# Kernel optimization log

Measured on AMD Instinct MI355X. Metric: run time of the kernel, lower is better.

The kernel has to match this reference:

```python
import jax, jax.numpy as jnp
import numpy as np

N = 20000
NNBR = 64
MESH = (64, 64, 64)
ORDER = 4          # B-spline interpolation order
ALPHA = 0.35       # Ewald splitting parameter (1/Angstrom)
BOX = 73.68        # cubic box edge (Angstrom)
KE = 14.399645478425668  # Coulomb constant, eV*Angstrom/e^2


def _Mn(x, n):
    """Cardinal B-spline M_n(x), support [0, n]."""
    if n == 2:
        return jnp.maximum(0.0, 1.0 - jnp.abs(x - 1.0))
    return (x * _Mn(x, n - 1) + (n - x) * _Mn(x - 1.0, n - 1)) / (n - 1)


def _bspline_fac(K):
    """|b(m)|^-2 ... i.e. 1/|Euler spline denominator|^2 per mesh dim."""
    m = jnp.arange(K, dtype=jnp.float32)
    k = jnp.arange(ORDER - 1, dtype=jnp.float32)
    Mv = _Mn(k + 1.0, ORDER)                       # M_n(1..n-1)
    phase = 2.0 * jnp.pi * m[:, None] * k[None, :] / K
    dre = jnp.sum(Mv * jnp.cos(phase), axis=1)
    dim = jnp.sum(Mv * jnp.sin(phase), axis=1)
    return 1.0 / (dre * dre + dim * dim)


def _pme_energy(positions, charges, cell, nbr, shifts):
    n = positions.shape[0]
    # ---------------- real-space short-range sum ----------------
    i_idx = jnp.arange(n)[:, None]
    valid = (nbr >= 0) & ~((nbr == i_idx) & jnp.all(shifts == 0, axis=-1))
    j = jnp.where(nbr >= 0, nbr, 0)
    rvec = positions[j] + shifts.astype(positions.dtype) @ cell - positions[:, None, :]
    r2 = jnp.sum(rvec * rvec, axis=-1)
    r = jnp.sqrt(jnp.where(valid, r2, 1.0))
    qq = charges[:, None] * charges[j]
    e_real = 0.5 * jnp.sum(jnp.where(valid, qq * jax.scipy.special.erfc(ALPHA * r) / r, 0.0))
    # ---------------- B-spline charge spreading ----------------
    Kx, Ky, Kz = MESH
    frac = positions @ jnp.linalg.inv(cell)        # cell rows = lattice vectors
    u = frac * jnp.array(MESH, dtype=positions.dtype)
    base = jnp.floor(u)
    t = u - base                                   # in [0, 1)
    basei = base.astype(jnp.int32)
    offs = jnp.arange(ORDER)
    wx = _Mn(t[:, 0:1] + offs, ORDER)              # [N, ORDER]
    wy = _Mn(t[:, 1:2] + offs, ORDER)
    wz = _Mn(t[:, 2:3] + offs, ORDER)
    ix = (basei[:, 0:1] - offs) % Kx
    iy = (basei[:, 1:2] - offs) % Ky
    iz = (basei[:, 2:3] - offs) % Kz
    W = (charges[:, None] * wx)[:, :, None, None] * wy[:, None, :, None] * wz[:, None, None, :]
    IDX = (ix[:, :, None, None] * Ky + iy[:, None, :, None]) * Kz + iz[:, None, None, :]
    mesh = jnp.zeros(Kx * Ky * Kz, positions.dtype).at[IDX.reshape(-1)].add(W.reshape(-1)).reshape(MESH)
    # ---------------- reciprocal-space FFT convolution ----------------
    Q = jnp.fft.fftn(mesh)
    Brec = 2.0 * jnp.pi * jnp.linalg.inv(cell).T   # rows are reciprocal vectors
    mx = (jnp.fft.fftfreq(Kx) * Kx).astype(positions.dtype)
    my = (jnp.fft.fftfreq(Ky) * Ky).astype(positions.dtype)
    mz = (jnp.fft.fftfreq(Kz) * Kz).astype(positions.dtype)
    kvec = (mx[:, None, None, None] * Brec[0] + my[None, :, None, None] * Brec[1]
            + mz[None, None, :, None] * Brec[2])
    k2 = jnp.sum(kvec * kvec, axis=-1)
    a2 = ALPHA * ALPHA
    kern = jnp.where(k2 > 0, jnp.exp(-k2 / (4.0 * a2)) / jnp.where(k2 > 0, k2, 1.0), 0.0)
    C = _bspline_fac(Kx)[:, None, None] * _bspline_fac(Ky)[None, :, None] * _bspline_fac(Kz)[None, None, :]
    vol = jnp.abs(jnp.linalg.det(cell))
    e_rec = (2.0 * jnp.pi / vol) * jnp.sum(kern * C * (Q.real ** 2 + Q.imag ** 2))
    # ---------------- self + neutralizing background ----------------
    qtot = jnp.sum(charges)
    e_self = -(ALPHA / jnp.sqrt(jnp.pi)) * jnp.sum(charges * charges)
    e_bg = -(jnp.pi / (2.0 * a2 * vol)) * qtot * qtot
    return e_real + e_rec + e_self + e_bg


def setup_inputs() -> dict:
    key = jax.random.key(0)
    k1, k2, k3 = jax.random.split(key, 3)
    positions = jax.random.uniform(k1, (N, 3), jnp.float32) * BOX
    q = jax.random.normal(k2, (N,), jnp.float32)
    q = q - jnp.mean(q)  # neutral system
    cell = BOX * jnp.eye(3, dtype=jnp.float32)
    nbr = jax.random.randint(k3, (N, NNBR), 0, N, jnp.int32)
    shifts = jnp.zeros((N, NNBR, 3), jnp.int32)
    return {"positions": positions, "node_charges": q, "cell": cell,
            "neighbor_matrix": nbr, "neighbor_shifts": shifts}


def reference(positions, node_charges, cell, neighbor_matrix, neighbor_shifts):
    def e_strain(pos, q, c, eps):
        F = jnp.eye(3, dtype=pos.dtype) + eps
        return _pme_energy(pos @ F, q, c @ F, neighbor_matrix, neighbor_shifts)

    eps0 = jnp.zeros((3, 3), positions.dtype)
    e, (g_pos, g_eps) = jax.value_and_grad(e_strain, argnums=(0, 3))(
        positions, node_charges, cell, eps0)
    vol = jnp.abs(jnp.linalg.det(cell))
    energies = e.reshape(1) * KE
    forces = -g_pos * KE
    virial = -0.5 * (g_eps + g_eps.T) * KE
    stresses = (virial / vol)[None]
    return energies, forces, stresses
```

## Files before the change

kernel.cpp:

```cpp
#include <hip/hip_runtime.h>
#include <math.h>

#define NATOM 20000
#define NNBR  64
#define KM    64
#define KM3   (KM*KM*KM)
#define NPAIR (NATOM*NNBR)

#define ALPHA_C 0.35f
#define KE_C    14.399645478425668f
#define TWO_OVER_SQRTPI 1.1283791670955126f
#define TWOPI_F 6.2831853071795864f
#define PI_F    3.14159265358979f
#define RC2     661.2244898f

#define WS_RE    0
#define WS_IM    (KM3)
#define WS_MESH  (2*KM3)
#define WS_GJ    (3*KM3)
#define WS_PART  (3*KM3 + 3*NATOM)
#define WS_FI    (WS_PART + 1024)
#define WS_POSQ  (WS_FI + 3*NATOM)
#define WS_NBS   (WS_POSQ + 4*NATOM)
#define ZERO_LEN (KM3 + 3*NATOM + 1024)

__device__ __forceinline__ float M2f(float x){ return fmaxf(0.f, 1.f - fabsf(x - 1.f)); }
__device__ __forceinline__ float M3f(float x){ return (x*M2f(x) + (3.f-x)*M2f(x-1.f)) * 0.5f; }
__device__ __forceinline__ float M4f(float x){ return (x*M3f(x) + (4.f-x)*M3f(x-1.f)) * (1.f/3.f); }

__device__ __forceinline__ float wsum64(float v){
#pragma unroll
  for(int off=32; off>0; off>>=1) v += __shfl_xor(v, off, 64);
  return v;
}

__device__ __forceinline__ float hinv9(const float* __restrict__ cell, float* h){
  float m00=cell[0],m01=cell[1],m02=cell[2];
  float m10=cell[3],m11=cell[4],m12=cell[5];
  float m20=cell[6],m21=cell[7],m22=cell[8];
  float det = m00*(m11*m22-m12*m21) - m01*(m10*m22-m12*m20) + m02*(m10*m21-m11*m20);
  float id = 1.f/det;
  h[0]=(m11*m22-m12*m21)*id; h[1]=(m02*m21-m01*m22)*id; h[2]=(m01*m12-m02*m11)*id;
  h[3]=(m12*m20-m10*m22)*id; h[4]=(m00*m22-m02*m20)*id; h[5]=(m02*m10-m00*m12)*id;
  h[6]=(m10*m21-m11*m20)*id; h[7]=(m01*m20-m00*m21)*id; h[8]=(m00*m11-m01*m10)*id;
  return fabsf(det);
}

__device__ __forceinline__ void fill_tw(int t, float* twr, float* twi){
  if(t < 64){
    float ss, cc; sincosf((TWOPI_F/64.f)*(float)t, &ss, &cc);
    twr[t] = cc; twi[t] = -ss;
  }
}

__device__ __forceinline__ void fft64t(float& xr, float& xi, int lane,
                                       const float* __restrict__ twr,
                                       const float* __restrict__ twi, float sgn){
#pragma unroll
  for(int k=0;k<6;k++){
    int half = 32 >> k;
    float or_ = __shfl_xor(xr, half, 64);
    float oi_ = __shfl_xor(xi, half, 64);
    bool hi = (lane & half) != 0;
    float sr = hi ? (or_ - xr) : (xr + or_);
    float si = hi ? (oi_ - xi) : (xi + oi_);
    int e = (lane & (half-1)) << k;
    float wr2 = hi ? twr[e] : 1.f;
    float wi2 = hi ? sgn*twi[e] : 0.f;
    xr = sr*wr2 - si*wi2;
    xi = sr*wi2 + si*wr2;
  }
  int rev = __brev((unsigned)lane) >> 26;
  xr = __shfl(xr, rev, 64);
  xi = __shfl(xi, rev, 64);
}

__global__ __launch_bounds__(256) void init_kernel(
    const float* __restrict__ pos, const float* __restrict__ q,
    const int* __restrict__ nbr, const int* __restrict__ shifts,
    float* __restrict__ zbase, float4* __restrict__ posq, int* __restrict__ nbs){
  int t = blockIdx.x*256 + threadIdx.x;
  if(t < ZERO_LEN) zbase[t] = 0.f;
  if(t < NATOM)
    posq[t] = make_float4(pos[3*t], pos[3*t+1], pos[3*t+2], q[t]);
  if(t < NPAIR){
    int j = nbr[t];
    int sx=shifts[3*t], sy=shifts[3*t+1], sz=shifts[3*t+2];
    int v;
    if(j < 0) v = -1;
    else v = (j & 0x7FFF) | ((sx+8)&15)<<15 | ((sy+8)&15)<<19 | ((sz+8)&15)<<23;
    nbs[t] = v;
  }
}

__global__ __launch_bounds__(256) void real_kernel(
    const float4* __restrict__ posq, const int* __restrict__ nbs,
    const float* __restrict__ cell,
    float* __restrict__ fi, float* __restrict__ gj, float* __restrict__ part){
  int lane = threadIdx.x & 63;
  int wid  = blockIdx.x*4 + (threadIdx.x>>6);
  int i0   = wid*4;
  float c0=cell[0],c1=cell[1],c2=cell[2];
  float c3=cell[3],c4=cell[4],c5=cell[5];
  float c6=cell[6],c7=cell[7],c8=cell[8];
  int v[4]; int jj[4]; float4 pi[4], pj[4];
#pragma unroll
  for(int k=0;k<4;k++) v[k]  = nbs[(i0+k)*NNBR + lane];
#pragma unroll
  for(int k=0;k<4;k++) pi[k] = posq[i0+k];
#pragma unroll
  for(int k=0;k<4;k++) jj[k] = min(v[k] & 0x7FFF, NATOM-1);
#pragma unroll
  for(int k=0;k<4;k++) pj[k] = posq[jj[k]];
  float e=0.f, vxx=0.f,vyy=0.f,vzz=0.f,vxy=0.f,vxz=0.f,vyz=0.f;
#pragma unroll
  for(int k=0;k<4;k++){
    int i = i0 + k;
    int vv = v[k], j = jj[k];
    int sx=((vv>>15)&15)-8, sy=((vv>>19)&15)-8, sz=((vv>>23)&15)-8;
    bool valid = (vv>=0) && !((j==i) && (sx==0) && (sy==0) && (sz==0));
    float rx = pj[k].x - pi[k].x + sx*c0 + sy*c3 + sz*c6;
    float ry = pj[k].y - pi[k].y + sx*c1 + sy*c4 + sz*c7;
    float rz = pj[k].z - pi[k].z + sx*c2 + sy*c5 + sz*c8;
    float r2 = rx*rx + ry*ry + rz*rz;
    float s = 0.f;
    if(valid && r2 > 0.f && r2 < RC2){
      float r = sqrtf(r2);
      float ar = ALPHA_C * r;
      float qq = pi[k].w * pj[k].w;
      float ef = erfcf(ar);
      float ex = expf(-ar*ar);
      float ir = 1.f/r;
      e += 0.5f*qq*ef*ir;
      s  = 0.5f*qq*(ef + TWO_OVER_SQRTPI*ar*ex)*ir*ir*ir;
    }
    float gx = s*rx, gy = s*ry, gz = s*rz;
    if(s != 0.f){
      unsafeAtomicAdd(&gj[3*j+0], -gx);
      unsafeAtomicAdd(&gj[3*j+1], -gy);
      unsafeAtomicAdd(&gj[3*j+2], -gz);
    }
    vxx -= s*rx*rx; vyy -= s*ry*ry; vzz -= s*rz*rz;
    vxy -= s*rx*ry; vxz -= s*rx*rz; vyz -= s*ry*rz;
    float tgx = wsum64(gx), tgy = wsum64(gy), tgz = wsum64(gz);
    if(lane==0){ fi[3*i]=tgx; fi[3*i+1]=tgy; fi[3*i+2]=tgz; }
  }
  e   = wsum64(e);
  vxx = wsum64(vxx); vyy = wsum64(vyy); vzz = wsum64(vzz);
  vxy = wsum64(vxy); vxz = wsum64(vxz); vyz = wsum64(vyz);
  if(lane==0){
    float* slot = part + (wid & 63)*16;
    unsafeAtomicAdd(&slot[0], e);
    unsafeAtomicAdd(&slot[1], vxx); unsafeAtomicAdd(&slot[2], vyy); unsafeAtomicAdd(&slot[3], vzz);
    unsafeAtomicAdd(&slot[4], vxy); unsafeAtomicAdd(&slot[5], vxz); unsafeAtomicAdd(&slot[6], vyz);
  }
}

__global__ __launch_bounds__(256) void spread_kernel(
    const float4* __restrict__ posq, const float* __restrict__ cell,
    float* __restrict__ mesh){
  int wid  = blockIdx.x*4 + (threadIdx.x>>6);
  int lane = threadIdx.x & 63;
  float h[9]; hinv9(cell, h);
  float4 pq = posq[wid];
  float u0=(pq.x*h[0]+pq.y*h[3]+pq.z*h[6])*(float)KM;
  float u1=(pq.x*h[1]+pq.y*h[4]+pq.z*h[7])*(float)KM;
  float u2=(pq.x*h[2]+pq.y*h[5]+pq.z*h[8])*(float)KM;
  float b0=floorf(u0), b1=floorf(u1), b2=floorf(u2);
  float t0=u0-b0, t1=u1-b1, t2=u2-b2;
  int i0=(int)b0, i1=(int)b1, i2=(int)b2;
  int a = lane>>4, b = (lane>>2)&3, c = lane&3;
  float w = pq.w * M4f(t0+(float)a) * M4f(t1+(float)b) * M4f(t2+(float)c);
  int ix=(i0-a+256)&63, iy=(i1-b+256)&63, iz=(i2-c+256)&63;
  unsafeAtomicAdd(&mesh[(ix*KM + iy)*KM + iz], w);
}

__global__ __launch_bounds__(256) void fftZF(const float* __restrict__ mesh,
                                             float* __restrict__ re, float* __restrict__ im){
  __shared__ float twr[64], twi[64];
  int t = threadIdx.x, lane = t&63;
  fill_tw(t, twr, twi);
  __syncthreads();
  int idx = blockIdx.x*256 + t;
  float xr = mesh[idx], xi = 0.f;
  fft64t(xr, xi, lane, twr, twi, 1.f);
  re[idx]=xr; im[idx]=xi;
}

__global__ __launch_bounds__(256) void fftZI(float* __restrict__ re, const float* __restrict__ im){
  __shared__ float twr[64], twi[64];
  int t = threadIdx.x, lane = t&63;
  fill_tw(t, twr, twi);
  __syncthreads();
  int idx = blockIdx.x*256 + t;
  float xr = re[idx], xi = im[idx];
  fft64t(xr, xi, lane, twr, twi, -1.f);
  re[idx]=xr;
}

__global__ __launch_bounds__(256) void fftY(float* __restrict__ re, float* __restrict__ im,
                                            float sgn){
  __shared__ float lr[64][17], li[64][17], twr[64], twi[64];
  int t = threadIdx.x, lane = t&63, w = t>>6;
  fill_tw(t, twr, twi);
  int x = blockIdx.x>>2, z0 = (blockIdx.x&3)*16;
  int off = x*4096 + z0;
#pragma unroll
  for(int k=0;k<4;k++){
    int e = k*256 + t; int y = e>>4, zz = e&15;
    lr[y][zz] = re[off + y*64 + zz];
    li[y][zz] = im[off + y*64 + zz];
  }
  __syncthreads();
#pragma unroll
  for(int qq=0; qq<4; qq++){
    int zz = w*4 + qq;
    float xr = lr[lane][zz], xi = li[lane][zz];
    fft64t(xr, xi, lane, twr, twi, sgn);
    lr[lane][zz] = xr; li[lane][zz] = xi;
  }
  __syncthreads();
#pragma unroll
  for(int k=0;k<4;k++){
    int e = k*256 + t; int y = e>>4, zz = e&15;
    re[off + y*64 + zz] = lr[y][zz];
    im[off + y*64 + zz] = li[y][zz];
  }
}

__global__ __launch_bounds__(256) void fftBC(float* __restrict__ re, float* __restrict__ im,
                                             const float* __restrict__ cell,
                                             float* __restrict__ part){
  __shared__ float lr[64][17], li[64][17], cf[64], twr[64], twi[64];
  int t = threadIdx.x, lane = t&63, w = t>>6;
  int y = blockIdx.x>>2, z0 = (blockIdx.x&3)*16;
  float h[9]; hinv9(cell, h);
  fill_tw(t, twr, twi);
  if(t < 64){
    float p1 = TWOPI_F*(float)t/64.f;
    float s1,c1_,s2,c2_; sincosf(p1,&s1,&c1_); sincosf(2.f*p1,&s2,&c2_);
    float dre = (1.f/6.f) + (2.f/3.f)*c1_ + (1.f/6.f)*c2_;
    float dim = (2.f/3.f)*s1 + (1.f/6.f)*s2;
    cf[t] = 1.f/(dre*dre + dim*dim);
  }
  float* rp = re + y*64 + z0;
  float* ip = im + y*64 + z0;
#pragma unroll
  for(int k=0;k<4;k++){
    int e = k*256 + t; int xI = e>>4, zz = e&15;
    lr[xI][zz] = rp[xI*4096 + zz];
    li[xI][zz] = ip[xI*4096 + zz];
  }
  __syncthreads();
  const float inv4a2 = 1.f/(4.f*ALPHA_C*ALPHA_C);
  float my_f = (float)((y<32)? y : y-64);
  float sE=0.f, v0=0.f,v1=0.f,v2=0.f,v3=0.f,v4=0.f,v5=0.f;
#pragma unroll
  for(int qq=0; qq<4; qq++){
    int zz = w*4 + qq; int z = z0 + zz;
    float xr = lr[lane][zz], xi = li[lane][zz];
    fft64t(xr, xi, lane, twr, twi, 1.f);
    int mx = lane, mz = z;
    float fx = (float)((mx<32)? mx : mx-64);
    float fz = (float)((mz<32)? mz : mz-64);
    float kx = TWOPI_F*(fx*h[0] + my_f*h[1] + fz*h[2]);
    float ky = TWOPI_F*(fx*h[3] + my_f*h[4] + fz*h[5]);
    float kz = TWOPI_F*(fx*h[6] + my_f*h[7] + fz*h[8]);
    float k2 = kx*kx + ky*ky + kz*kz;
    float wk = 0.f;
    if(k2 > 0.f){
      float kern = expf(-k2*inv4a2)/k2;
      wk = kern * cf[mx]*cf[y]*cf[z];
      float q2 = xr*xr + xi*xi;
      sE += wk*q2;
      float fac = wk*q2*(inv4a2 + 1.f/k2)*2.f;
      v0 += fac*kx*kx; v1 += fac*ky*ky; v2 += fac*kz*kz;
      v3 += fac*kx*ky; v4 += fac*kx*kz; v5 += fac*ky*kz;
    }
    xr *= wk; xi *= wk;
    fft64t(xr, xi, lane, twr, twi, -1.f);
    lr[lane][zz] = xr; li[lane][zz] = xi;
  }
  __syncthreads();
#pragma unroll
  for(int k=0;k<4;k++){
    int e = k*256 + t; int xI = e>>4, zz = e&15;
    rp[xI*4096 + zz] = lr[xI][zz];
    ip[xI*4096 + zz] = li[xI][zz];
  }
  sE = wsum64(sE);
  v0 = wsum64(v0); v1 = wsum64(v1); v2 = wsum64(v2);
  v3 = wsum64(v3); v4 = wsum64(v4); v5 = wsum64(v5);
  if(lane==0){
    float* slot = part + (((blockIdx.x<<2)|w)&63)*16;
    unsafeAtomicAdd(&slot[7],  sE);
    unsafeAtomicAdd(&slot[8],  v0); unsafeAtomicAdd(&slot[9],  v1);
    unsafeAtomicAdd(&slot[10], v2); unsafeAtomicAdd(&slot[11], v3);
    unsafeAtomicAdd(&slot[12], v4); unsafeAtomicAdd(&slot[13], v5);
  }
}

__global__ __launch_bounds__(256) void gather_kernel(
    const float4* __restrict__ posq, const float* __restrict__ cell,
    const float* __restrict__ phi,
    const float* __restrict__ fi, const float* __restrict__ gj,
    const float* __restrict__ part, float* __restrict__ out){
  __shared__ float sa[256], sb[256], facc[16];
  int wid  = blockIdx.x*4 + (threadIdx.x>>6);
  int lane = threadIdx.x & 63;
  float h[9]; float V = hinv9(cell, h);
  float4 pq = posq[wid];
  float u0=(pq.x*h[0]+pq.y*h[3]+pq.z*h[6])*(float)KM;
  float u1=(pq.x*h[1]+pq.y*h[4]+pq.z*h[7])*(float)KM;
  float u2=(pq.x*h[2]+pq.y*h[5]+pq.z*h[8])*(float)KM;
  float b0=floorf(u0), b1=floorf(u1), b2=floorf(u2);
  float t0=u0-b0, t1=u1-b1, t2=u2-b2;
  int i0=(int)b0, i1=(int)b1, i2=(int)b2;
  int a = lane>>4, b = (lane>>2)&3, c = lane&3;
  float fa=(float)a, fb=(float)b, fc=(float)c;
  float wxa=M4f(t0+fa), wyb=M4f(t1+fb), wzc=M4f(t2+fc);
  float dxa=M3f(t0+fa)-M3f(t0+fa-1.f);
  float dyb=M3f(t1+fb)-M3f(t1+fb-1.f);
  float dzc=M3f(t2+fc)-M3f(t2+fc-1.f);
  int ix=(i0-a+256)&63, iy=(i1-b+256)&63, iz=(i2-c+256)&63;
  float p = phi[(ix*KM + iy)*KM + iz];
  float Sx = wsum64(p*dxa*wyb*wzc);
  float Sy = wsum64(p*wxa*dyb*wzc);
  float Sz = wsum64(p*wxa*wyb*dzc);
  if(lane==0){
    float scale = pq.w * (2.f*TWOPI_F/V) * (float)KM;
    float g0 = scale*(Sx*h[0] + Sy*h[1] + Sz*h[2]);
    float g1 = scale*(Sx*h[3] + Sy*h[4] + Sz*h[5]);
    float g2 = scale*(Sx*h[6] + Sy*h[7] + Sz*h[8]);
    out[1+3*wid+0] = -KE_C*(fi[3*wid+0] + gj[3*wid+0] + g0);
    out[1+3*wid+1] = -KE_C*(fi[3*wid+1] + gj[3*wid+1] + g1);
    out[1+3*wid+2] = -KE_C*(fi[3*wid+2] + gj[3*wid+2] + g2);
  }
  if(blockIdx.x==0){
    int t = threadIdx.x;
    float qa=0.f, qb=0.f;
    for(int i=t;i<NATOM;i+=256){ float qv=posq[i].w; qa+=qv; qb+=qv*qv; }
    sa[t]=qa; sb[t]=qb; __syncthreads();
    for(int off=128; off>0; off>>=1){
      if(t<off){ sa[t]+=sa[t+off]; sb[t]+=sb[t+off]; } __syncthreads();
    }
    if(t<14){ float s=0.f; for(int sl=0;sl<64;sl++) s+=part[sl*16+t]; facc[t]=s; }
    __syncthreads();
    if(t==0){
      float qtot = sa[0], sumq2 = sb[0];
      float a2 = ALPHA_C*ALPHA_C;
      float pref = TWOPI_F/V;
      float e_real = facc[0];
      float e_rec  = pref*facc[7];
      float e_self = -(ALPHA_C/sqrtf(PI_F))*sumq2;
      float e_bg   = -(PI_F/(2.f*a2*V))*qtot*qtot;
      out[0] = (e_real + e_rec + e_self + e_bg)*KE_C;
      float gxx = facc[1] + pref*facc[8]  - e_rec - e_bg;
      float gyy = facc[2] + pref*facc[9]  - e_rec - e_bg;
      float gzz = facc[3] + pref*facc[10] - e_rec - e_bg;
      float gxy = facc[4] + pref*facc[11];
      float gxz = facc[5] + pref*facc[12];
      float gyz = facc[6] + pref*facc[13];
      float cc = -KE_C/V;
      float* st = out + 1 + 3*NATOM;
      st[0]=cc*gxx; st[4]=cc*gyy; st[8]=cc*gzz;
      st[1]=cc*gxy; st[3]=cc*gxy;
      st[2]=cc*gxz; st[6]=cc*gxz;
      st[5]=cc*gyz; st[7]=cc*gyz;
    }
  }
}

extern "C" void kernel_launch(void* const* d_in, const int* in_sizes, int n_in,
                              void* d_out, int out_size, void* d_ws, size_t ws_size,
                              hipStream_t stream) {
  const float* pos  = (const float*)d_in[0];
  const float* q    = (const float*)d_in[1];
  const float* cell = (const float*)d_in[2];
  const int* nbr    = (const int*)d_in[3];
  const int* shifts = (const int*)d_in[4];
  float* out = (float*)d_out;
  float* ws  = (float*)d_ws;
  float*  bufRe = ws + WS_RE;
  float*  bufIm = ws + WS_IM;
  float*  mesh  = ws + WS_MESH;
  float*  gj    = ws + WS_GJ;
  float*  part  = ws + WS_PART;
  float*  fi    = ws + WS_FI;
  float4* posq  = (float4*)(ws + WS_POSQ);
  int*    nbs   = (int*)(ws + WS_NBS);

  init_kernel<<<(NPAIR+255)/256,256,0,stream>>>(pos, q, nbr, shifts, mesh, posq, nbs);
  real_kernel<<<1250,256,0,stream>>>(posq, nbs, cell, fi, gj, part);
  spread_kernel<<<5000,256,0,stream>>>(posq, cell, mesh);
  fftZF<<<1024,256,0,stream>>>(mesh, bufRe, bufIm);
  fftY <<< 256,256,0,stream>>>(bufRe, bufIm, 1.f);
  fftBC<<< 256,256,0,stream>>>(bufRe, bufIm, cell, part);
  fftY <<< 256,256,0,stream>>>(bufRe, bufIm, -1.f);
  fftZI<<<1024,256,0,stream>>>(bufRe, bufIm);
  gather_kernel<<<5000,256,0,stream>>>(posq, cell, bufRe, fi, gj, part, out);
}
```

Measured before the change: 185.6 us.

## Merge real-space and spreading kernels; gather four atoms per wavefront

The real-space pair kernel and the B-spline charge-spreading kernel become one launch: the first 1250 blocks do pair work and the remaining 5000 blocks spread charges, so the two independent phases can run concurrently and one launch is removed. The gather kernel now handles four atoms per wavefront, issuing their mesh loads together before the reductions to expose more memory-level parallelism, and it launches 1250 blocks instead of 5000. The cost is a divergent branch and higher register pressure in the fused kernel, plus fewer gather blocks. Block 0 of gather still computes the global energy/stress sums.

```diff
diff --git a/kernel.cpp b/kernel.cpp
--- a/kernel.cpp
+++ b/kernel.cpp
@@ -93,86 +93,84 @@
   }
 }
 
-__global__ __launch_bounds__(256) void real_kernel(
+__global__ __launch_bounds__(256) void realspread_kernel(
     const float4* __restrict__ posq, const int* __restrict__ nbs,
     const float* __restrict__ cell,
-    float* __restrict__ fi, float* __restrict__ gj, float* __restrict__ part){
+    float* __restrict__ fi, float* __restrict__ gj, float* __restrict__ part,
+    float* __restrict__ mesh){
   int lane = threadIdx.x & 63;
-  int wid  = blockIdx.x*4 + (threadIdx.x>>6);
-  int i0   = wid*4;
-  float c0=cell[0],c1=cell[1],c2=cell[2];
-  float c3=cell[3],c4=cell[4],c5=cell[5];
-  float c6=cell[6],c7=cell[7],c8=cell[8];
-  int v[4]; int jj[4]; float4 pi[4], pj[4];
-#pragma unroll
-  for(int k=0;k<4;k++) v[k]  = nbs[(i0+k)*NNBR + lane];
-#pragma unroll
-  for(int k=0;k<4;k++) pi[k] = posq[i0+k];
-#pragma unroll
-  for(int k=0;k<4;k++) jj[k] = min(v[k] & 0x7FFF, NATOM-1);
-#pragma unroll
-  for(int k=0;k<4;k++) pj[k] = posq[jj[k]];
-  float e=0.f, vxx=0.f,vyy=0.f,vzz=0.f,vxy=0.f,vxz=0.f,vyz=0.f;
-#pragma unroll
-  for(int k=0;k<4;k++){
-    int i = i0 + k;
-    int vv = v[k], j = jj[k];
-    int sx=((vv>>15)&15)-8, sy=((vv>>19)&15)-8, sz=((vv>>23)&15)-8;
-    bool valid = (vv>=0) && !((j==i) && (sx==0) && (sy==0) && (sz==0));
-    float rx = pj[k].x - pi[k].x + sx*c0 + sy*c3 + sz*c6;
-    float ry = pj[k].y - pi[k].y + sx*c1 + sy*c4 + sz*c7;
-    float rz = pj[k].z - pi[k].z + sx*c2 + sy*c5 + sz*c8;
-    float r2 = rx*rx + ry*ry + rz*rz;
-    float s = 0.f;
-    if(valid && r2 > 0.f && r2 < RC2){
-      float r = sqrtf(r2);
-      float ar = ALPHA_C * r;
-      float qq = pi[k].w * pj[k].w;
-      float ef = erfcf(ar);
-      float ex = expf(-ar*ar);
-      float ir = 1.f/r;
-      e += 0.5f*qq*ef*ir;
-      s  = 0.5f*qq*(ef + TWO_OVER_SQRTPI*ar*ex)*ir*ir*ir;
-    }
-    float gx = s*rx, gy = s*ry, gz = s*rz;
-    if(s != 0.f){
-      unsafeAtomicAdd(&gj[3*j+0], -gx);
-      unsafeAtomicAdd(&gj[3*j+1], -gy);
-      unsafeAtomicAdd(&gj[3*j+2], -gz);
-    }
-    vxx -= s*rx*rx; vyy -= s*ry*ry; vzz -= s*rz*rz;
-    vxy -= s*rx*ry; vxz -= s*rx*rz; vyz -= s*ry*rz;
-    float tgx = wsum64(gx), tgy = wsum64(gy), tgz = wsum64(gz);
-    if(lane==0){ fi[3*i]=tgx; fi[3*i+1]=tgy; fi[3*i+2]=tgz; }
-  }
-  e   = wsum64(e);
-  vxx = wsum64(vxx); vyy = wsum64(vyy); vzz = wsum64(vzz);
-  vxy = wsum64(vxy); vxz = wsum64(vxz); vyz = wsum64(vyz);
-  if(lane==0){
-    float* slot = part + (wid & 63)*16;
-    unsafeAtomicAdd(&slot[0], e);
-    unsafeAtomicAdd(&slot[1], vxx); unsafeAtomicAdd(&slot[2], vyy); unsafeAtomicAdd(&slot[3], vzz);
-    unsafeAtomicAdd(&slot[4], vxy); unsafeAtomicAdd(&slot[5], vxz); unsafeAtomicAdd(&slot[6], vyz);
-  }
-}
-
-__global__ __launch_bounds__(256) void spread_kernel(
-    const float4* __restrict__ posq, const float* __restrict__ cell,
-    float* __restrict__ mesh){
-  int wid  = blockIdx.x*4 + (threadIdx.x>>6);
-  int lane = threadIdx.x & 63;
-  float h[9]; hinv9(cell, h);
-  float4 pq = posq[wid];
-  float u0=(pq.x*h[0]+pq.y*h[3]+pq.z*h[6])*(float)KM;
-  float u1=(pq.x*h[1]+pq.y*h[4]+pq.z*h[7])*(float)KM;
-  float u2=(pq.x*h[2]+pq.y*h[5]+pq.z*h[8])*(float)KM;
-  float b0=floorf(u0), b1=floorf(u1), b2=floorf(u2);
-  float t0=u0-b0, t1=u1-b1, t2=u2-b2;
-  int i0=(int)b0, i1=(int)b1, i2=(int)b2;
-  int a = lane>>4, b = (lane>>2)&3, c = lane&3;
-  float w = pq.w * M4f(t0+(float)a) * M4f(t1+(float)b) * M4f(t2+(float)c);
-  int ix=(i0-a+256)&63, iy=(i1-b+256)&63, iz=(i2-c+256)&63;
-  unsafeAtomicAdd(&mesh[(ix*KM + iy)*KM + iz], w);
+  if(blockIdx.x < 1250){
+    int wid  = blockIdx.x*4 + (threadIdx.x>>6);
+    int i0   = wid*4;
+    float c0=cell[0],c1=cell[1],c2=cell[2];
+    float c3=cell[3],c4=cell[4],c5=cell[5];
+    float c6=cell[6],c7=cell[7],c8=cell[8];
+    int v[4]; int jj[4]; float4 pi[4], pj[4];
+#pragma unroll
+    for(int k=0;k<4;k++) v[k]  = nbs[(i0+k)*NNBR + lane];
+#pragma unroll
+    for(int k=0;k<4;k++) pi[k] = posq[i0+k];
+#pragma unroll
+    for(int k=0;k<4;k++) jj[k] = min(v[k] & 0x7FFF, NATOM-1);
+#pragma unroll
+    for(int k=0;k<4;k++) pj[k] = posq[jj[k]];
+    float e=0.f, vxx=0.f,vyy=0.f,vzz=0.f,vxy=0.f,vxz=0.f,vyz=0.f;
+#pragma unroll
+    for(int k=0;k<4;k++){
+      int i = i0 + k;
+      int vv = v[k], j = jj[k];
+      int sx=((vv>>15)&15)-8, sy=((vv>>19)&15)-8, sz=((vv>>23)&15)-8;
+      bool valid = (vv>=0) && !((j==i) && (sx==0) && (sy==0) && (sz==0));
+      float rx = pj[k].x - pi[k].x + sx*c0 + sy*c3 + sz*c6;
+      float ry = pj[k].y - pi[k].y + sx*c1 + sy*c4 + sz*c7;
+      float rz = pj[k].z - pi[k].z + sx*c2 + sy*c5 + sz*c8;
+      float r2 = rx*rx + ry*ry + rz*rz;
+      float s = 0.f;
+      if(valid && r2 > 0.f && r2 < RC2){
+        float r = sqrtf(r2);
+        float ar = ALPHA_C * r;
+        float qq = pi[k].w * pj[k].w;
+        float ef = erfcf(ar);
+        float ex = expf(-ar*ar);
+        float ir = 1.f/r;
+        e += 0.5f*qq*ef*ir;
+        s  = 0.5f*qq*(ef + TWO_OVER_SQRTPI*ar*ex)*ir*ir*ir;
+      }
+      float gx = s*rx, gy = s*ry, gz = s*rz;
+      if(s != 0.f){
+        unsafeAtomicAdd(&gj[3*j+0], -gx);
+        unsafeAtomicAdd(&gj[3*j+1], -gy);
+        unsafeAtomicAdd(&gj[3*j+2], -gz);
+      }
+      vxx -= s*rx*rx; vyy -= s*ry*ry; vzz -= s*rz*rz;
+      vxy -= s*rx*ry; vxz -= s*rx*rz; vyz -= s*ry*rz;
+      float tgx = wsum64(gx), tgy = wsum64(gy), tgz = wsum64(gz);
+      if(lane==0){ fi[3*i]=tgx; fi[3*i+1]=tgy; fi[3*i+2]=tgz; }
+    }
+    e   = wsum64(e);
+    vxx = wsum64(vxx); vyy = wsum64(vyy); vzz = wsum64(vzz);
+    vxy = wsum64(vxy); vxz = wsum64(vxz); vyz = wsum64(vyz);
+    if(lane==0){
+      float* slot = part + (wid & 63)*16;
+      unsafeAtomicAdd(&slot[0], e);
+      unsafeAtomicAdd(&slot[1], vxx); unsafeAtomicAdd(&slot[2], vyy); unsafeAtomicAdd(&slot[3], vzz);
+      unsafeAtomicAdd(&slot[4], vxy); unsafeAtomicAdd(&slot[5], vxz); unsafeAtomicAdd(&slot[6], vyz);
+    }
+  } else {
+    int wid = (blockIdx.x - 1250)*4 + (threadIdx.x>>6);
+    float h[9]; hinv9(cell, h);
+    float4 pq = posq[wid];
+    float u0=(pq.x*h[0]+pq.y*h[3]+pq.z*h[6])*(float)KM;
+    float u1=(pq.x*h[1]+pq.y*h[4]+pq.z*h[7])*(float)KM;
+    float u2=(pq.x*h[2]+pq.y*h[5]+pq.z*h[8])*(float)KM;
+    float b0=floorf(u0), b1=floorf(u1), b2=floorf(u2);
+    float t0=u0-b0, t1=u1-b1, t2=u2-b2;
+    int i0=(int)b0, i1=(int)b1, i2=(int)b2;
+    int a = lane>>4, b = (lane>>2)&3, c = lane&3;
+    float w = pq.w * M4f(t0+(float)a) * M4f(t1+(float)b) * M4f(t2+(float)c);
+    int ix=(i0-a+256)&63, iy=(i1-b+256)&63, iz=(i2-c+256)&63;
+    unsafeAtomicAdd(&mesh[(ix*KM + iy)*KM + iz], w);
+  }
 }
 
 __global__ __launch_bounds__(256) void fftZF(const float* __restrict__ mesh,
@@ -306,35 +304,45 @@
     const float* __restrict__ fi, const float* __restrict__ gj,
     const float* __restrict__ part, float* __restrict__ out){
   __shared__ float sa[256], sb[256], facc[16];
+  int lane = threadIdx.x & 63;
   int wid  = blockIdx.x*4 + (threadIdx.x>>6);
-  int lane = threadIdx.x & 63;
+  int i0   = wid*4;
   float h[9]; float V = hinv9(cell, h);
-  float4 pq = posq[wid];
-  float u0=(pq.x*h[0]+pq.y*h[3]+pq.z*h[6])*(float)KM;
-  float u1=(pq.x*h[1]+pq.y*h[4]+pq.z*h[7])*(float)KM;
-  float u2=(pq.x*h[2]+pq.y*h[5]+pq.z*h[8])*(float)KM;
-  float b0=floorf(u0), b1=floorf(u1), b2=floorf(u2);
-  float t0=u0-b0, t1=u1-b1, t2=u2-b2;
-  int i0=(int)b0, i1=(int)b1, i2=(int)b2;
   int a = lane>>4, b = (lane>>2)&3, c = lane&3;
   float fa=(float)a, fb=(float)b, fc=(float)c;
-  float wxa=M4f(t0+fa), wyb=M4f(t1+fb), wzc=M4f(t2+fc);
-  float dxa=M3f(t0+fa)-M3f(t0+fa-1.f);
-  float dyb=M3f(t1+fb)-M3f(t1+fb-1.f);
-  float dzc=M3f(t2+fc)-M3f(t2+fc-1.f);
-  int ix=(i0-a+256)&63, iy=(i1-b+256)&63, iz=(i2-c+256)&63;
-  float p = phi[(ix*KM + iy)*KM + iz];
-  float Sx = wsum64(p*dxa*wyb*wzc);
-  float Sy = wsum64(p*wxa*dyb*wzc);
-  float Sz = wsum64(p*wxa*wyb*dzc);
-  if(lane==0){
-    float scale = pq.w * (2.f*TWOPI_F/V) * (float)KM;
-    float g0 = scale*(Sx*h[0] + Sy*h[1] + Sz*h[2]);
-    float g1 = scale*(Sx*h[3] + Sy*h[4] + Sz*h[5]);
-    float g2 = scale*(Sx*h[6] + Sy*h[7] + Sz*h[8]);
-    out[1+3*wid+0] = -KE_C*(fi[3*wid+0] + gj[3*wid+0] + g0);
-    out[1+3*wid+1] = -KE_C*(fi[3*wid+1] + gj[3*wid+1] + g1);
-    out[1+3*wid+2] = -KE_C*(fi[3*wid+2] + gj[3*wid+2] + g2);
+  float4 pq[4];
+#pragma unroll
+  for(int k=0;k<4;k++) pq[k] = posq[i0+k];
+  float t0[4], t1[4], t2[4]; float p[4];
+#pragma unroll
+  for(int k=0;k<4;k++){
+    float u0=(pq[k].x*h[0]+pq[k].y*h[3]+pq[k].z*h[6])*(float)KM;
+    float u1=(pq[k].x*h[1]+pq[k].y*h[4]+pq[k].z*h[7])*(float)KM;
+    float u2=(pq[k].x*h[2]+pq[k].y*h[5]+pq[k].z*h[8])*(float)KM;
+    float b0=floorf(u0), b1=floorf(u1), b2=floorf(u2);
+    t0[k]=u0-b0; t1[k]=u1-b1; t2[k]=u2-b2;
+    int ix=((int)b0-a+256)&63, iy=((int)b1-b+256)&63, iz=((int)b2-c+256)&63;
+    p[k] = phi[(ix*KM + iy)*KM + iz];
+  }
+#pragma unroll
+  for(int k=0;k<4;k++){
+    float wxa=M4f(t0[k]+fa), wyb=M4f(t1[k]+fb), wzc=M4f(t2[k]+fc);
+    float dxa=M3f(t0[k]+fa)-M3f(t0[k]+fa-1.f);
+    float dyb=M3f(t1[k]+fb)-M3f(t1[k]+fb-1.f);
+    float dzc=M3f(t2[k]+fc)-M3f(t2[k]+fc-1.f);
+    float Sx = wsum64(p[k]*dxa*wyb*wzc);
+    float Sy = wsum64(p[k]*wxa*dyb*wzc);
+    float Sz = wsum64(p[k]*wxa*wyb*dzc);
+    if(lane==0){
+      int i = i0 + k;
+      float scale = pq[k].w * (2.f*TWOPI_F/V) * (float)KM;
+      float g0 = scale*(Sx*h[0] + Sy*h[1] + Sz*h[2]);
+      float g1 = scale*(Sx*h[3] + Sy*h[4] + Sz*h[5]);
+      float g2 = scale*(Sx*h[6] + Sy*h[7] + Sz*h[8]);
+      out[1+3*i+0] = -KE_C*(fi[3*i+0] + gj[3*i+0] + g0);
+      out[1+3*i+1] = -KE_C*(fi[3*i+1] + gj[3*i+1] + g1);
+      out[1+3*i+2] = -KE_C*(fi[3*i+2] + gj[3*i+2] + g2);
+    }
   }
   if(blockIdx.x==0){
     int t = threadIdx.x;
@@ -391,12 +399,11 @@
   int*    nbs   = (int*)(ws + WS_NBS);
 
   init_kernel<<<(NPAIR+255)/256,256,0,stream>>>(pos, q, nbr, shifts, mesh, posq, nbs);
-  real_kernel<<<1250,256,0,stream>>>(posq, nbs, cell, fi, gj, part);
-  spread_kernel<<<5000,256,0,stream>>>(posq, cell, mesh);
+  realspread_kernel<<<6250,256,0,stream>>>(posq, nbs, cell, fi, gj, part, mesh);
   fftZF<<<1024,256,0,stream>>>(mesh, bufRe, bufIm);
   fftY <<< 256,256,0,stream>>>(bufRe, bufIm, 1.f);
   fftBC<<< 256,256,0,stream>>>(bufRe, bufIm, cell, part);
   fftY <<< 256,256,0,stream>>>(bufRe, bufIm, -1.f);
   fftZI<<<1024,256,0,stream>>>(bufRe, bufIm);
-  gather_kernel<<<5000,256,0,stream>>>(posq, cell, bufRe, fi, gj, part, out);
-}
+  gather_kernel<<<1250,256,0,stream>>>(posq, cell, bufRe, fi, gj, part, out);
+}
```

After: 179.8 us. -3.1%, faster.
